# Performance work log

Measured on AMD Instinct MI355X. Metric: run time of the kernel, lower is better.

The kernel has to match this reference:

```python
import jax, jax.numpy as jnp
import numpy as np

E, H, F = 8, 1024, 4096  # experts, hidden_size, ffn_hidden_size
INIT_STD = 0.02


def setup_inputs() -> dict:
    key = jax.random.key(0)
    kx, k1, k2 = jax.random.split(key, 3)
    total_tokens = 16384
    x = jax.random.normal(kx, (total_tokens, H), dtype=jnp.float32)
    w1 = jax.random.normal(k1, (E, H, F), dtype=jnp.float32) * INIT_STD
    w2 = jax.random.normal(k2, (E, F, H), dtype=jnp.float32) * INIT_STD
    return {"x": x, "w1": w1, "w2": w2, "rows_per_expert": total_tokens // E}


def reference(x, w1, w2, rows_per_expert):
    # Grouped GEMM 1: per-expert x_e @ w1[e]  -> [E, T, F]
    e, h = w1.shape[0], w1.shape[1]
    xg = x.reshape(e, rows_per_expert, h)          # tokens grouped by expert
    inter = jnp.einsum('eth,ehf->etf', xg, w1)     # grouped GEMM 1
    inter = jax.nn.gelu(inter)                     # activation_fn
    out = jnp.einsum('etf,efh->eth', inter, w2)    # grouped GEMM 2
    return out.reshape(-1, h)
```

## Files before the change

### kernel.cpp

```cpp
#include <hip/hip_runtime.h>
#include <hip/hip_bf16.h>


typedef __attribute__((ext_vector_type(8))) short short8;
typedef __attribute__((ext_vector_type(4))) float floatx4;

static __device__ __forceinline__ ushort f2bf(float f) {
  __hip_bfloat16 h = __float2bfloat16(f);
  return *(ushort*)&h;
}

static __device__ __forceinline__ int swz(int n, int o) {
  return o ^ (n & 7) ^ ((n >> 3) & 7);
}

template<int K, int N>
static __device__ __forceinline__ void tpose_tile(const float* __restrict__ in,
                                                  __hip_bfloat16* __restrict__ out,
                                                  ushort* lds, int e, int nt, int kt) {
  const size_t eoff = (size_t)e * K * N;
  const int n0 = nt * 128, k0 = kt * 64;
  const int t = threadIdx.x;
  const int j = t & 15;
  const int g = t >> 4;
  const int o = g >> 1;
  const int h = g & 1;
  const float* src = in + eoff + (size_t)(k0 + 8 * o) * N + n0 + h * 64 + 4 * j;
  float4 v[8];
#pragma unroll
  for (int r = 0; r < 8; ++r)
    v[r] = *(const float4*)(src + (size_t)r * N);
#pragma unroll
  for (int i = 0; i < 4; ++i) {
    const int n = h * 64 + 4 * j + i;
    union { short8 s8; ushort u[8]; } p;
#pragma unroll
    for (int r = 0; r < 8; ++r)
      p.u[r] = f2bf(((const float*)&v[r])[i]);
    *(short8*)(lds + n * 64 + swz(n, o) * 8) = p.s8;
  }
  __syncthreads();
  const int c = t & 7;
  const int r0 = t >> 3;
#pragma unroll
  for (int p = 0; p < 4; ++p) {
    const int n = p * 32 + r0;
    short8 u = *(const short8*)(lds + n * 64 + swz(n, c) * 8);
    *(short8*)(out + eoff + (size_t)(n0 + n) * K + k0 + 8 * c) = u;
  }
}

static __device__ __forceinline__ void cvt_part(const float* __restrict__ x,
                                                __hip_bfloat16* __restrict__ xb, int b) {
  const int t = threadIdx.x;
  const float4* src = (const float4*)x + (size_t)b * 2048 + t;
  ushort4* dst = (ushort4*)xb + (size_t)b * 2048 + t;
#pragma unroll
  for (int u = 0; u < 8; ++u) {
    float4 v = src[u * 256];
    ushort4 q;
    q.x = f2bf(v.x); q.y = f2bf(v.y); q.z = f2bf(v.z); q.w = f2bf(v.w);
    dst[u * 256] = q;
  }
}

__global__ __launch_bounds__(256) void prep(const float* __restrict__ x,
                                            const float* __restrict__ w1,
                                            const float* __restrict__ w2,
                                            __hip_bfloat16* __restrict__ xb,
                                            __hip_bfloat16* __restrict__ w1t,
                                            __hip_bfloat16* __restrict__ w2t) {
  __shared__ __align__(16) ushort lds[128 * 64];
  const int b = blockIdx.x;
  if (b < 2048) {
    cvt_part(x, xb, b);
  } else if (b < 6144) {
    const int bb = b - 2048;
    tpose_tile<1024, 4096>(w1, w1t, lds, bb >> 9, bb & 31, (bb >> 5) & 15);
  } else {
    const int bb = b - 6144;
    tpose_tile<4096, 1024>(w2, w2t, lds, bb >> 9, bb & 7, (bb >> 3) & 63);
  }
}

template<bool GELU, typename OutT>
__global__ __launch_bounds__(256) void gemm_bt(const __hip_bfloat16* __restrict__ A,
                                               const __hip_bfloat16* __restrict__ Bt,
                                               OutT* __restrict__ C,
                                               int M, int N, int K) {
  __shared__ __align__(16) __hip_bfloat16 As[128 * 32];
  __shared__ __align__(16) __hip_bfloat16 Bs[128 * 32];

  const int e = blockIdx.z;
  A  += (size_t)e * M * K;
  Bt += (size_t)e * N * K;
  C  += (size_t)e * M * N;

  const int m0 = blockIdx.y * 128;
  const int n0 = blockIdx.x * 128;
  const int t = threadIdx.x;
  const int lane = t & 63;
  const int l16 = lane & 15;
  const int quad = lane >> 4;
  const int w = t >> 6;
  const int wr = (w >> 1) * 64;
  const int wc = (w & 1) * 64;

  floatx4 acc[4][4] = {};

  for (int k0 = 0; k0 < K; k0 += 32) {
    __syncthreads();
#pragma unroll
    for (int i = 0; i < 2; ++i) {
      const int id = t + i * 256;
      const int row = id >> 2;
      const int cc = (id & 3) * 8;
      __builtin_amdgcn_global_load_lds(
          (const __attribute__((address_space(1))) void*)(A + (size_t)(m0 + row) * K + k0 + cc),
          (__attribute__((address_space(3))) void*)(As + id * 8), 16, 0, 0);
    }
#pragma unroll
    for (int i = 0; i < 2; ++i) {
      const int id = t + i * 256;
      const int row = id >> 2;
      const int cc = (id & 3) * 8;
      __builtin_amdgcn_global_load_lds(
          (const __attribute__((address_space(1))) void*)(Bt + (size_t)(n0 + row) * K + k0 + cc),
          (__attribute__((address_space(3))) void*)(Bs + id * 8), 16, 0, 0);
    }
    __syncthreads();

    short8 af[4], bf[4];
#pragma unroll
    for (int i = 0; i < 4; ++i)
      af[i] = *(const short8*)(As + (wr + i * 16 + l16) * 32 + quad * 8);
#pragma unroll
    for (int j = 0; j < 4; ++j)
      bf[j] = *(const short8*)(Bs + (wc + j * 16 + l16) * 32 + quad * 8);
#pragma unroll
    for (int i = 0; i < 4; ++i)
#pragma unroll
      for (int j = 0; j < 4; ++j)
        acc[i][j] = __builtin_amdgcn_mfma_f32_16x16x32_bf16(af[i], bf[j], acc[i][j], 0, 0, 0);
  }

#pragma unroll
  for (int i = 0; i < 4; ++i) {
#pragma unroll
    for (int r = 0; r < 4; ++r) {
      const int row = m0 + wr + i * 16 + quad * 4 + r;
      OutT* crow = C + (size_t)row * N + n0 + wc + l16;
#pragma unroll
      for (int j = 0; j < 4; ++j) {
        float v = acc[i][j][r];
        if constexpr (GELU) {
          const float u2 = 1.5957691216057308f * (v + 0.044715f * v * v * v);
          const float ex = __expf(u2);
          v = v - v * __builtin_amdgcn_rcpf(ex + 1.0f);
        }
        if constexpr (sizeof(OutT) == 2)
          crow[j * 16] = __float2bfloat16(v);
        else
          crow[j * 16] = v;
      }
    }
  }
}

extern "C" void kernel_launch(void* const* d_in, const int* in_sizes, int n_in,
                              void* d_out, int out_size, void* d_ws, size_t ws_size,
                              hipStream_t stream) {
  const float* x  = (const float*)d_in[0];
  const float* w1 = (const float*)d_in[1];
  const float* w2 = (const float*)d_in[2];
  float* out = (float*)d_out;

  char* ws = (char*)d_ws;
  __hip_bfloat16* xb    = (__hip_bfloat16*)(ws);
  __hip_bfloat16* w1t   = (__hip_bfloat16*)(ws + (size_t)32 * 1024 * 1024);
  __hip_bfloat16* w2t   = (__hip_bfloat16*)(ws + (size_t)96 * 1024 * 1024);
  __hip_bfloat16* inter = (__hip_bfloat16*)(ws + (size_t)160 * 1024 * 1024);

  prep<<<10240, 256, 0, stream>>>(x, w1, w2, xb, w1t, w2t);
  gemm_bt<true, __hip_bfloat16>
      <<<dim3(32, 16, 8), 256, 0, stream>>>(xb, w1t, inter, 2048, 4096, 1024);
  gemm_bt<false, float>
      <<<dim3(8, 16, 8), 256, 0, stream>>>(inter, w2t, out, 2048, 1024, 4096);
}
```

Baseline: 754.7 us.

## Replace GEMM with 256x256-tile 8-wave kernel using multi-stage LDS pipeline

Swaps the simple 128x128 single-buffered GEMM for a 256x256-tile, 512-thread kernel. It uses a multi-stage LDS ring of 64-wide K slices with async global-to-LDS loads interleaved between MFMA phases, an XOR swizzle to avoid LDS bank conflicts, raised scheduling priority around the MFMAs, and an XCD-aware block remap. The aim is to hide memory latency, raise data reuse per tile and improve L2 locality. In exchange it uses a large shared buffer, relies on hand-placed waitcnt and barriers, and launches fewer blocks, which may limit occupancy on the smaller second GEMM.

```diff
diff --git a/kernel.cpp b/kernel.cpp
--- a/kernel.cpp
+++ b/kernel.cpp
@@ -9,6 +9,7 @@
   __hip_bfloat16 h = __float2bfloat16(f);
   return *(ushort*)&h;
 }
+
 
 static __device__ __forceinline__ int swz(int n, int o) {
   return o ^ (n & 7) ^ ((n >> 3) & 7);
@@ -83,73 +84,189 @@
   }
 }
 
+
+#define GLDS16(src, dst)                                                       \
+  __builtin_amdgcn_global_load_lds(                                            \
+      (const __attribute__((address_space(1))) void*)(src),                    \
+      (__attribute__((address_space(3))) void*)(dst), 16, 0, 0)
+
+#define WAITVM(n) asm volatile("s_waitcnt vmcnt(" #n ")" ::: "memory")
+
+#define MFMA16(a, b, c) __builtin_amdgcn_mfma_f32_16x16x32_bf16(a, b, c, 0, 0, 0)
+
+static __device__ __forceinline__ void barsync() {
+  asm volatile("" ::: "memory");
+  __builtin_amdgcn_sched_barrier(0);
+  __builtin_amdgcn_s_barrier();
+  __builtin_amdgcn_sched_barrier(0);
+  asm volatile("" ::: "memory");
+}
+
+template<int C>
+static __device__ __forceinline__ void ktile(
+    int kt, int nt, int t,
+    const __hip_bfloat16* __restrict__ aread, const __hip_bfloat16* __restrict__ bread,
+    const __hip_bfloat16* __restrict__ Asrc0, const __hip_bfloat16* __restrict__ Asrc1,
+    const __hip_bfloat16* __restrict__ Bsrc0, const __hip_bfloat16* __restrict__ Bsrc1,
+    __hip_bfloat16* As, __hip_bfloat16* Bs,
+    floatx4 (&acc)[8][4]) {
+  const int kc1 = (kt + 1) * 64 + 32;
+  const int kc2 = (kt + 2) * 64;
+  const bool st1 = (kt + 1 < nt);
+  const bool st2 = (kt + 2 < nt);
+  short8 af[4], bf[4];
+
+#pragma unroll
+  for (int i = 0; i < 4; ++i)
+    af[i] = *(const short8*)(aread + (C * 2 + 0) * 8192 + i * 512);
+#pragma unroll
+  for (int j = 0; j < 4; ++j)
+    bf[j] = *(const short8*)(bread + (C * 2 + 0) * 8192 + j * 512);
+  if (st1) {
+    __hip_bfloat16* d = As + ((C ^ 1) * 2 + 1) * 8192;
+    GLDS16(Asrc0 + kc1, d + t * 8);
+    GLDS16(Asrc1 + kc1, d + 4096 + t * 8);
+  }
+  barsync();
+  __builtin_amdgcn_s_setprio(1);
+#pragma unroll
+  for (int i = 0; i < 4; ++i)
+#pragma unroll
+    for (int j = 0; j < 4; ++j)
+      acc[i][j] = MFMA16(af[i], bf[j], acc[i][j]);
+  __builtin_amdgcn_s_setprio(0);
+  barsync();
+
+#pragma unroll
+  for (int i = 0; i < 4; ++i)
+    af[i] = *(const short8*)(aread + (C * 2 + 0) * 8192 + 2048 + i * 512);
+  if (st1) {
+    __hip_bfloat16* d = Bs + ((C ^ 1) * 2 + 1) * 8192;
+    GLDS16(Bsrc0 + kc1, d + t * 8);
+    GLDS16(Bsrc1 + kc1, d + 4096 + t * 8);
+  }
+  barsync();
+  __builtin_amdgcn_s_setprio(1);
+#pragma unroll
+  for (int i = 0; i < 4; ++i)
+#pragma unroll
+    for (int j = 0; j < 4; ++j)
+      acc[i + 4][j] = MFMA16(af[i], bf[j], acc[i + 4][j]);
+  __builtin_amdgcn_s_setprio(0);
+  barsync();
+
+#pragma unroll
+  for (int i = 0; i < 4; ++i)
+    af[i] = *(const short8*)(aread + (C * 2 + 1) * 8192 + i * 512);
+#pragma unroll
+  for (int j = 0; j < 4; ++j)
+    bf[j] = *(const short8*)(bread + (C * 2 + 1) * 8192 + j * 512);
+  if (st2) {
+    __hip_bfloat16* d = As + (C * 2 + 0) * 8192;
+    GLDS16(Asrc0 + kc2, d + t * 8);
+    GLDS16(Asrc1 + kc2, d + 4096 + t * 8);
+  }
+  barsync();
+  __builtin_amdgcn_s_setprio(1);
+#pragma unroll
+  for (int i = 0; i < 4; ++i)
+#pragma unroll
+    for (int j = 0; j < 4; ++j)
+      acc[i][j] = MFMA16(af[i], bf[j], acc[i][j]);
+  __builtin_amdgcn_s_setprio(0);
+  barsync();
+
+#pragma unroll
+  for (int i = 0; i < 4; ++i)
+    af[i] = *(const short8*)(aread + (C * 2 + 1) * 8192 + 2048 + i * 512);
+  if (st2) {
+    __hip_bfloat16* d = Bs + (C * 2 + 0) * 8192;
+    GLDS16(Bsrc0 + kc2, d + t * 8);
+    GLDS16(Bsrc1 + kc2, d + 4096 + t * 8);
+  }
+  barsync();
+  __builtin_amdgcn_s_setprio(1);
+#pragma unroll
+  for (int i = 0; i < 4; ++i)
+#pragma unroll
+    for (int j = 0; j < 4; ++j)
+      acc[i + 4][j] = MFMA16(af[i], bf[j], acc[i + 4][j]);
+  __builtin_amdgcn_s_setprio(0);
+  if (st2) { WAITVM(4); } else { WAITVM(0); }
+  barsync();
+}
+
 template<bool GELU, typename OutT>
-__global__ __launch_bounds__(256) void gemm_bt(const __hip_bfloat16* __restrict__ A,
-                                               const __hip_bfloat16* __restrict__ Bt,
-                                               OutT* __restrict__ C,
-                                               int M, int N, int K) {
-  __shared__ __align__(16) __hip_bfloat16 As[128 * 32];
-  __shared__ __align__(16) __hip_bfloat16 Bs[128 * 32];
+__global__ __launch_bounds__(512, 2) void gemm8(
+    const __hip_bfloat16* __restrict__ A, const __hip_bfloat16* __restrict__ Bt,
+    OutT* __restrict__ C, int M, int N, int K) {
+  __shared__ __align__(16) __hip_bfloat16 lds[65536];
+  __hip_bfloat16* As = lds;
+  __hip_bfloat16* Bs = lds + 32768;
 
   const int e = blockIdx.z;
   A  += (size_t)e * M * K;
   Bt += (size_t)e * N * K;
   C  += (size_t)e * M * N;
 
-  const int m0 = blockIdx.y * 128;
-  const int n0 = blockIdx.x * 128;
+  const int MT = M >> 8, NT = N >> 8;
+  const int lin = blockIdx.x;
+  const int xcd = lin & 7;
+  const int idx = lin >> 3;
+  const int mh = MT >> 1, nq = NT >> 2;
+  const int mt  = (xcd >> 2) * mh + idx % mh;
+  const int nti = (xcd & 3) * nq + idx / mh;
+  const int m0 = mt << 8, n0 = nti << 8;
+
   const int t = threadIdx.x;
   const int lane = t & 63;
   const int l16 = lane & 15;
   const int quad = lane >> 4;
   const int w = t >> 6;
-  const int wr = (w >> 1) * 64;
-  const int wc = (w & 1) * 64;
-
-  floatx4 acc[4][4] = {};
-
-  for (int k0 = 0; k0 < K; k0 += 32) {
-    __syncthreads();
-#pragma unroll
-    for (int i = 0; i < 2; ++i) {
-      const int id = t + i * 256;
-      const int row = id >> 2;
-      const int cc = (id & 3) * 8;
-      __builtin_amdgcn_global_load_lds(
-          (const __attribute__((address_space(1))) void*)(A + (size_t)(m0 + row) * K + k0 + cc),
-          (__attribute__((address_space(3))) void*)(As + id * 8), 16, 0, 0);
-    }
-#pragma unroll
-    for (int i = 0; i < 2; ++i) {
-      const int id = t + i * 256;
-      const int row = id >> 2;
-      const int cc = (id & 3) * 8;
-      __builtin_amdgcn_global_load_lds(
-          (const __attribute__((address_space(1))) void*)(Bt + (size_t)(n0 + row) * K + k0 + cc),
-          (__attribute__((address_space(3))) void*)(Bs + id * 8), 16, 0, 0);
-    }
-    __syncthreads();
-
-    short8 af[4], bf[4];
-#pragma unroll
-    for (int i = 0; i < 4; ++i)
-      af[i] = *(const short8*)(As + (wr + i * 16 + l16) * 32 + quad * 8);
-#pragma unroll
-    for (int j = 0; j < 4; ++j)
-      bf[j] = *(const short8*)(Bs + (wc + j * 16 + l16) * 32 + quad * 8);
-#pragma unroll
-    for (int i = 0; i < 4; ++i)
-#pragma unroll
-      for (int j = 0; j < 4; ++j)
-        acc[i][j] = __builtin_amdgcn_mfma_f32_16x16x32_bf16(af[i], bf[j], acc[i][j], 0, 0, 0);
-  }
-
-#pragma unroll
-  for (int i = 0; i < 4; ++i) {
+  const int wr = w >> 2;
+  const int wc = w & 3;
+  const int sx = (quad ^ ((l16 >> 1) & 3)) * 8;
+
+  const __hip_bfloat16* aread = As + (wr * 128 + l16) * 32 + sx;
+  const __hip_bfloat16* bread = Bs + (wc * 64 + l16) * 32 + sx;
+
+  const int r0s = t >> 2;
+  const int q0s = ((t & 3) ^ ((r0s >> 1) & 3)) * 8;
+  const int r1s = r0s + 128;
+  const int q1s = ((t & 3) ^ ((r1s >> 1) & 3)) * 8;
+  const __hip_bfloat16* Asrc0 = A  + (size_t)(m0 + r0s) * K + q0s;
+  const __hip_bfloat16* Asrc1 = A  + (size_t)(m0 + r1s) * K + q1s;
+  const __hip_bfloat16* Bsrc0 = Bt + (size_t)(n0 + r0s) * K + q0s;
+  const __hip_bfloat16* Bsrc1 = Bt + (size_t)(n0 + r1s) * K + q1s;
+
+  const int nt = K >> 6;
+  floatx4 acc[8][4] = {};
+
+  GLDS16(Asrc0 + 0,  As + t * 8);            GLDS16(Asrc1 + 0,  As + 4096 + t * 8);
+  GLDS16(Bsrc0 + 0,  Bs + t * 8);            GLDS16(Bsrc1 + 0,  Bs + 4096 + t * 8);
+  GLDS16(Asrc0 + 32, As + 8192 + t * 8);     GLDS16(Asrc1 + 32, As + 12288 + t * 8);
+  GLDS16(Bsrc0 + 32, Bs + 8192 + t * 8);     GLDS16(Bsrc1 + 32, Bs + 12288 + t * 8);
+  if (nt > 1) {
+    GLDS16(Asrc0 + 64, As + 16384 + t * 8);  GLDS16(Asrc1 + 64, As + 20480 + t * 8);
+    GLDS16(Bsrc0 + 64, Bs + 16384 + t * 8);  GLDS16(Bsrc1 + 64, Bs + 20480 + t * 8);
+    WAITVM(4);
+  } else {
+    WAITVM(0);
+  }
+  barsync();
+
+  for (int kt = 0; kt < nt; kt += 2) {
+    ktile<0>(kt,     nt, t, aread, bread, Asrc0, Asrc1, Bsrc0, Bsrc1, As, Bs, acc);
+    ktile<1>(kt + 1, nt, t, aread, bread, Asrc0, Asrc1, Bsrc0, Bsrc1, As, Bs, acc);
+  }
+
+  const int mrow = m0 + wr * 128 + quad * 4;
+  const int ncol = n0 + wc * 64 + l16;
+#pragma unroll
+  for (int i = 0; i < 8; ++i) {
 #pragma unroll
     for (int r = 0; r < 4; ++r) {
-      const int row = m0 + wr + i * 16 + quad * 4 + r;
-      OutT* crow = C + (size_t)row * N + n0 + wc + l16;
+      OutT* crow = C + (size_t)(mrow + i * 16 + r) * N + ncol;
 #pragma unroll
       for (int j = 0; j < 4; ++j) {
         float v = acc[i][j][r];
@@ -182,8 +299,8 @@
   __hip_bfloat16* inter = (__hip_bfloat16*)(ws + (size_t)160 * 1024 * 1024);
 
   prep<<<10240, 256, 0, stream>>>(x, w1, w2, xb, w1t, w2t);
-  gemm_bt<true, __hip_bfloat16>
-      <<<dim3(32, 16, 8), 256, 0, stream>>>(xb, w1t, inter, 2048, 4096, 1024);
-  gemm_bt<false, float>
-      <<<dim3(8, 16, 8), 256, 0, stream>>>(inter, w2t, out, 2048, 1024, 4096);
-}
+  gemm8<true, __hip_bfloat16>
+      <<<dim3(128, 1, 8), 512, 0, stream>>>(xb, w1t, inter, 2048, 4096, 1024);
+  gemm8<false, float>
+      <<<dim3(32, 1, 8), 512, 0, stream>>>(inter, w2t, out, 2048, 1024, 4096);
+}
```

New measurement: 619.6 us. 17.9% less time.
